# Kernel optimization log

Hardware: AMD Instinct MI355X
Metric: run time of the kernel (lower is better)

Reference implementation:

```python
import jax, jax.numpy as jnp
import numpy as np

NUM_GROUPS = 32
EPS = 1e-5


def setup_inputs() -> dict:
    key = jax.random.key(0)
    k1, k2, k3 = jax.random.split(key, 3)
    B, C, H, W = 16, 768, 32, 32
    x = jax.random.normal(k1, (B, C, H, W), dtype=jnp.float32)
    # 1x1-conv weights, scaled ~1/sqrt(fan_in) so softmax logits are sane
    w_qkv = jax.random.normal(k2, (3 * C, C), dtype=jnp.float32) / np.sqrt(C)
    b_qkv = jnp.zeros((3 * C,), dtype=jnp.float32)
    w_out = jax.random.normal(k3, (C, C), dtype=jnp.float32) / np.sqrt(C)
    b_out = jnp.zeros((C,), dtype=jnp.float32)
    gn_gamma = jnp.ones((C,), dtype=jnp.float32)
    gn_beta = jnp.zeros((C,), dtype=jnp.float32)
    return {"x": x, "gn_gamma": gn_gamma, "gn_beta": gn_beta,
            "w_qkv": w_qkv, "b_qkv": b_qkv, "w_out": w_out, "b_out": b_out}


def _group_norm(x, gamma, beta):
    B, C, H, W = x.shape
    G = NUM_GROUPS
    xr = x.reshape(B, G, C // G, H, W)
    mean = xr.mean(axis=(2, 3, 4), keepdims=True)
    var = xr.var(axis=(2, 3, 4), keepdims=True)  # biased, matches torch GroupNorm
    xn = ((xr - mean) * jax.lax.rsqrt(var + EPS)).reshape(B, C, H, W)
    return xn * gamma[None, :, None, None] + beta[None, :, None, None]


def reference(x, gn_gamma, gn_beta, w_qkv, b_qkv, w_out, b_out):
    B, C, H, W = x.shape
    res = x
    xn = _group_norm(x, gn_gamma, gn_beta)
    # 1x1 conv == channel GEMM: [B,3C,H,W]
    qkv = jnp.einsum('bchw,oc->bohw', xn, w_qkv) + b_qkv[None, :, None, None]
    q, k, v = jnp.split(qkv, 3, axis=1)
    hw = H * W
    q = q.reshape(B, C, hw)
    k = k.reshape(B, C, hw)
    v = v.reshape(B, C, hw)
    scale = hw ** -0.5
    # attention over the channel axis (C is 'seq len', hw is feature dim)
    att = jnp.einsum('bid,bjd->bij', q, k) * scale  # [B, C, C]
    att = jax.nn.softmax(att, axis=-1)
    # dropout p = 0.0 -> identity
    out = jnp.einsum('bij,bjd->bid', att, v).reshape(B, C, H, W)
    out = jnp.einsum('bchw,oc->bohw', out, w_out) + b_out[None, :, None, None]
    return out + res
```

## Files before the change

kernel.cpp:

```cpp
#include <hip/hip_runtime.h>
#include <hip/hip_bf16.h>

#define HW 1024
#define C_CH 768
#define BATCH 16
#define NG 32
#define CPG 24
#define EPS 1e-5f

typedef __attribute__((ext_vector_type(8))) short bf16x8;
typedef __attribute__((ext_vector_type(4))) float f32x4;
typedef unsigned short u16;
typedef unsigned int u32;

typedef const __attribute__((address_space(1))) void* gas_ptr;
typedef __attribute__((address_space(3))) void* las_ptr;

__device__ __forceinline__ void load_lds16(const void* g, void* l) {
    __builtin_amdgcn_global_load_lds((gas_ptr)g, (las_ptr)l, 16, 0, 0);
}

__device__ __forceinline__ u16 f2bf(float f) {
    __hip_bfloat16 h = __float2bfloat16(f);
    return *(u16*)&h;
}
__device__ __forceinline__ float bf2f(u16 u) {
    return __uint_as_float(((u32)u) << 16);
}

__device__ __forceinline__ void xcd_remap(int& bx, int& by, int& bz) {
    const int nbx = gridDim.x, nby = gridDim.y;
    const int nwg = nbx * nby * gridDim.z;
    int bid = blockIdx.x + nbx * (blockIdx.y + nby * blockIdx.z);
    if ((nwg & 7) == 0) {
        const int q = nwg >> 3;
        bid = (bid & 7) * q + (bid >> 3);
    }
    bx = bid % nbx;
    int t2 = bid / nbx;
    by = t2 % nby;
    bz = t2 / nby;
}

__global__ __launch_bounds__(256) void cast_bf16_kernel(const float4* __restrict__ in,
                                                        ushort4* __restrict__ out, int n4) {
    int i = blockIdx.x * 256 + threadIdx.x;
    if (i >= n4) return;
    float4 v = in[i];
    ushort4 u;
    u.x = f2bf(v.x); u.y = f2bf(v.y); u.z = f2bf(v.z); u.w = f2bf(v.w);
    out[i] = u;
}

__global__ __launch_bounds__(256) void gn_stats_kernel(const float* __restrict__ x,
                                                       float* __restrict__ stats) {
    int bg = blockIdx.x;
    const float4* p4 = (const float4*)(x + (size_t)bg * (CPG * HW));
    float s = 0.f, s2 = 0.f;
    for (int i = threadIdx.x; i < (CPG * HW) / 4; i += 256) {
        float4 v = p4[i];
        s  += v.x + v.y + v.z + v.w;
        s2 += v.x * v.x + v.y * v.y + v.z * v.z + v.w * v.w;
    }
    int lane = threadIdx.x & 63, wid = threadIdx.x >> 6;
    for (int off = 32; off; off >>= 1) {
        s  += __shfl_xor(s,  off, 64);
        s2 += __shfl_xor(s2, off, 64);
    }
    __shared__ float red[8];
    if (lane == 0) { red[wid * 2] = s; red[wid * 2 + 1] = s2; }
    __syncthreads();
    if (threadIdx.x == 0) {
        s = red[0] + red[2] + red[4] + red[6];
        s2 = red[1] + red[3] + red[5] + red[7];
        float mean = s / (float)(CPG * HW);
        float var  = s2 / (float)(CPG * HW) - mean * mean;
        stats[2 * bg]     = mean;
        stats[2 * bg + 1] = rsqrtf(var + EPS);
    }
}

__global__ __launch_bounds__(256) void gn_norm_kernel(const float* __restrict__ x,
                                                      const float* __restrict__ stats,
                                                      const float* __restrict__ gamma,
                                                      const float* __restrict__ beta,
                                                      __hip_bfloat16* __restrict__ xnT) {
    __shared__ float lds[64][65];
    int b  = blockIdx.y;
    int p0 = blockIdx.x * 64;
    int t = threadIdx.x;
    int lane = t & 63;
    int grp  = t >> 6;
    for (int cc = 0; cc < C_CH / 64; cc++) {
        int c0 = cc * 64;
        for (int i = 0; i < 16; i++) {
            int c = c0 + grp * 16 + i;
            float2 st = ((const float2*)stats)[b * NG + c / CPG];
            float ga = gamma[c], be = beta[c];
            float v = x[((size_t)b * C_CH + c) * HW + p0 + lane];
            lds[lane][grp * 16 + i] = (v - st.x) * st.y * ga + be;
        }
        __syncthreads();
        for (int i = 0; i < 16; i++) {
            int pp = grp * 16 + i;
            xnT[((size_t)b * HW + p0 + pp) * C_CH + c0 + lane] =
                __float2bfloat16(lds[pp][lane]);
        }
        __syncthreads();
    }
}

__global__ __launch_bounds__(256) void softmax_kernel(__hip_bfloat16* __restrict__ att) {
    int row  = blockIdx.x * 4 + (threadIdx.x >> 6);
    int lane = threadIdx.x & 63;
    u16* p = (u16*)(att + (size_t)row * C_CH);
    float v[12];
    float m = -1e30f;
    for (int j = 0; j < 12; j++) {
        v[j] = bf2f(p[j * 64 + lane]);
        m = fmaxf(m, v[j]);
    }
    for (int off = 32; off; off >>= 1) m = fmaxf(m, __shfl_xor(m, off, 64));
    float s = 0.f;
    for (int j = 0; j < 12; j++) { v[j] = __expf(v[j] - m); s += v[j]; }
    for (int off = 32; off; off >>= 1) s += __shfl_xor(s, off, 64);
    float inv = 1.0f / s;
    for (int j = 0; j < 12; j++) p[j * 64 + lane] = f2bf(v[j] * inv);
}

template<int OUT_F32>
__global__ __launch_bounds__(256, 2) void gemm_nt_kernel(
    const __hip_bfloat16* __restrict__ A, long sA,
    const __hip_bfloat16* __restrict__ B, long sB,
    void* __restrict__ Cout, long sC, int ldc,
    int K, float scale,
    const float* __restrict__ bias_row,
    const float* __restrict__ bias_col,
    const float* __restrict__ residual, long sR)
{
    __shared__ __hip_bfloat16 ldsA[128 * 64];
    __shared__ __hip_bfloat16 ldsB[128 * 64];
    int bxx, byy, bzz;
    xcd_remap(bxx, byy, bzz);
    const int t  = threadIdx.x;
    const int b  = bzz;
    const int m0 = byy * 128;
    const int n0 = bxx * 128;
    const int lane = t & 63;
    const int wid  = t >> 6;
    const int wm = wid >> 1, wn = wid & 1;
    const int lrow = lane & 15, lk = lane >> 4;

    const int srow   = t >> 3;
    const int schunk = t & 7;
    const int kphys  = (schunk ^ (srow & 7)) * 8;

    const __hip_bfloat16* aBase = A + (size_t)b * sA + (size_t)(m0 + srow) * K + kphys;
    const __hip_bfloat16* bBase = B + (size_t)b * sB + (size_t)(n0 + srow) * K + kphys;
    const int ldsDst = (t & ~63) * 8;

    f32x4 acc[4][4] = {};

    const int nk = K >> 6;
    for (int kt = 0; kt < nk; kt++) {
        __syncthreads();
        const __hip_bfloat16* ak = aBase + (size_t)kt * 64;
        const __hip_bfloat16* bk = bBase + (size_t)kt * 64;
        for (int r = 0; r < 4; r++)
            load_lds16(ak + (size_t)r * 32 * K, &ldsA[ldsDst + r * 2048]);
        for (int r = 0; r < 4; r++)
            load_lds16(bk + (size_t)r * 32 * K, &ldsB[ldsDst + r * 2048]);
        __syncthreads();
        for (int h = 0; h < 2; h++) {
            bf16x8 af[4], bfr[4];
            const int lc = h * 4 + lk;
            for (int i = 0; i < 4; i++) {
                int row = wm * 64 + i * 16 + lrow;
                int pc = lc ^ (row & 7);
                af[i] = *(const bf16x8*)&ldsA[row * 64 + pc * 8];
            }
            for (int i = 0; i < 4; i++) {
                int col = wn * 64 + i * 16 + lrow;
                int pc = lc ^ (col & 7);
                bfr[i] = *(const bf16x8*)&ldsB[col * 64 + pc * 8];
            }
            for (int i = 0; i < 4; i++)
                for (int j = 0; j < 4; j++)
                    acc[i][j] = __builtin_amdgcn_mfma_f32_16x16x32_bf16(
                        af[i], bfr[j], acc[i][j], 0, 0, 0);
        }
    }

    __hip_bfloat16* outB = (__hip_bfloat16*)Cout;
    float* outF = (float*)Cout;
    for (int i = 0; i < 4; i++)
        for (int j = 0; j < 4; j++) {
            int row = m0 + wm * 64 + i * 16 + lk * 4;
            int col = n0 + wn * 64 + j * 16 + lrow;
            f32x4 a = acc[i][j];
            for (int r = 0; r < 4; r++) {
                int rr = row + r;
                float v = a[r] * scale;
                if (bias_row) v += bias_row[rr];
                if (bias_col) v += bias_col[col];
                if (residual) v += residual[(size_t)b * sR + (size_t)rr * ldc + col];
                size_t off = (size_t)b * sC + (size_t)rr * ldc + col;
                if (OUT_F32) outF[off] = v;
                else         outB[off] = __float2bfloat16(v);
            }
        }
}

__global__ __launch_bounds__(512, 2) void gemm_nt_qkv(
    const __hip_bfloat16* __restrict__ A,
    const __hip_bfloat16* __restrict__ B, long sB,
    __hip_bfloat16* __restrict__ Cout, long sC, int ldc,
    int K,
    const float* __restrict__ bias_row,
    __hip_bfloat16* __restrict__ vt_out, long sVT, int vt_start)
{
    __shared__ __hip_bfloat16 ldsA[256 * 64];
    __shared__ __hip_bfloat16 ldsB[128 * 64];
    int bxx, byy, bzz;
    xcd_remap(bxx, byy, bzz);
    const int t  = threadIdx.x;
    const int b  = bzz;
    const int m0 = byy * 256;
    const int n0 = bxx * 128;
    const int lane = t & 63;
    const int wid  = t >> 6;
    const int wm = wid >> 1;
    const int wn = wid & 1;
    const int lrow = lane & 15, lk = lane >> 4;

    const int srow  = t >> 3;
    const int kphys = ((t & 7) ^ (srow & 7)) * 8;
    const int dstW  = (t & ~63) * 8;

    const __hip_bfloat16* aBase = A + (size_t)(m0 + srow) * K + kphys;
    const __hip_bfloat16* bBase = B + (size_t)b * sB + (size_t)(n0 + srow) * K + kphys;

    f32x4 acc[4][4] = {};

    const int nk = K >> 6;
    for (int kt = 0; kt < nk; kt++) {
        __syncthreads();
        const __hip_bfloat16* ak = aBase + (size_t)kt * 64;
        const __hip_bfloat16* bk = bBase + (size_t)kt * 64;
#pragma unroll
        for (int l = 0; l < 4; l++)
            load_lds16(ak + (size_t)l * 64 * K, &ldsA[dstW + l * 4096]);
#pragma unroll
        for (int l = 0; l < 2; l++)
            load_lds16(bk + (size_t)l * 64 * K, &ldsB[dstW + l * 4096]);
        __syncthreads();
#pragma unroll
        for (int h = 0; h < 2; h++) {
            bf16x8 af[4], bfr[4];
            const int lc = h * 4 + lk;
#pragma unroll
            for (int i = 0; i < 4; i++) {
                int row = wm * 64 + i * 16 + lrow;
                af[i] = *(const bf16x8*)&ldsA[row * 64 + (lc ^ (row & 7)) * 8];
            }
#pragma unroll
            for (int j = 0; j < 4; j++) {
                int col = wn * 64 + j * 16 + lrow;
                bfr[j] = *(const bf16x8*)&ldsB[col * 64 + (lc ^ (col & 7)) * 8];
            }
#pragma unroll
            for (int i = 0; i < 4; i++)
#pragma unroll
                for (int j = 0; j < 4; j++)
                    acc[i][j] = __builtin_amdgcn_mfma_f32_16x16x32_bf16(
                        af[i], bfr[j], acc[i][j], 0, 0, 0);
        }
    }

    if (m0 >= vt_start) {
        __hip_bfloat16* vtp = vt_out + (size_t)b * sVT;
#pragma unroll
        for (int i = 0; i < 4; i++)
#pragma unroll
            for (int j = 0; j < 4; j++) {
                int row = m0 + wm * 64 + i * 16 + lk * 4;
                int col = n0 + wn * 64 + j * 16 + lrow;
                f32x4 a = acc[i][j];
                ushort4 u;
                u.x = f2bf(a[0] + bias_row[row + 0]);
                u.y = f2bf(a[1] + bias_row[row + 1]);
                u.z = f2bf(a[2] + bias_row[row + 2]);
                u.w = f2bf(a[3] + bias_row[row + 3]);
                *(ushort4*)(vtp + (size_t)col * C_CH + (row - vt_start)) = u;
            }
        return;
    }

#pragma unroll
    for (int i = 0; i < 4; i++)
#pragma unroll
        for (int j = 0; j < 4; j++) {
            int row = m0 + wm * 64 + i * 16 + lk * 4;
            int col = n0 + wn * 64 + j * 16 + lrow;
            f32x4 a = acc[i][j];
#pragma unroll
            for (int r = 0; r < 4; r++) {
                int rr = row + r;
                Cout[(size_t)b * sC + (size_t)rr * ldc + col] =
                    __float2bfloat16(a[r] + bias_row[rr]);
            }
        }
}

extern "C" void kernel_launch(void* const* d_in, const int* in_sizes, int n_in,
                              void* d_out, int out_size, void* d_ws, size_t ws_size,
                              hipStream_t stream) {
    const float* x     = (const float*)d_in[0];
    const float* gamma = (const float*)d_in[1];
    const float* beta  = (const float*)d_in[2];
    const float* w_qkv = (const float*)d_in[3];
    const float* b_qkv = (const float*)d_in[4];
    const float* w_out = (const float*)d_in[5];
    const float* b_out = (const float*)d_in[6];

    char* ws = (char*)d_ws;
    size_t off = 0;
    auto alloc = [&](size_t bytes) {
        void* p = ws + off;
        off += (bytes + 255) & ~(size_t)255;
        return p;
    };
    __hip_bfloat16* xnT   = (__hip_bfloat16*)alloc((size_t)BATCH * HW * C_CH * 2);
    __hip_bfloat16* wqkvB = (__hip_bfloat16*)alloc((size_t)3 * C_CH * C_CH * 2);
    __hip_bfloat16* woutB = (__hip_bfloat16*)alloc((size_t)C_CH * C_CH * 2);
    __hip_bfloat16* qk    = (__hip_bfloat16*)alloc((size_t)BATCH * 2 * C_CH * HW * 2);
    __hip_bfloat16* vT    = (__hip_bfloat16*)alloc((size_t)BATCH * HW * C_CH * 2);
    __hip_bfloat16* att   = (__hip_bfloat16*)alloc((size_t)BATCH * C_CH * C_CH * 2);
    __hip_bfloat16* outT  = (__hip_bfloat16*)alloc((size_t)BATCH * HW * C_CH * 2);
    float* stats          = (float*)alloc((size_t)BATCH * NG * 2 * 4);

    {
        int n4 = (3 * C_CH * C_CH) / 4;
        cast_bf16_kernel<<<(n4 + 255) / 256, 256, 0, stream>>>(
            (const float4*)w_qkv, (ushort4*)wqkvB, n4);
        int n4b = (C_CH * C_CH) / 4;
        cast_bf16_kernel<<<(n4b + 255) / 256, 256, 0, stream>>>(
            (const float4*)w_out, (ushort4*)woutB, n4b);
    }
    gn_stats_kernel<<<BATCH * NG, 256, 0, stream>>>(x, stats);
    gn_norm_kernel<<<dim3(HW / 64, BATCH), 256, 0, stream>>>(x, stats, gamma, beta, xnT);

    gemm_nt_qkv<<<dim3(HW / 128, 2304 / 256, BATCH), 512, 0, stream>>>(
        wqkvB, xnT, (long)HW * C_CH, qk, (long)2 * C_CH * HW, HW,
        C_CH, b_qkv, vT, (long)HW * C_CH, 2 * C_CH);

    gemm_nt_kernel<0><<<dim3(C_CH / 128, C_CH / 128, BATCH), 256, 0, stream>>>(
        qk, (long)2 * C_CH * HW, qk + (size_t)C_CH * HW, (long)2 * C_CH * HW,
        att, (long)C_CH * C_CH, C_CH,
        HW, 1.0f / 32.0f, nullptr, nullptr, nullptr, 0);

    softmax_kernel<<<(BATCH * C_CH) / 4, 256, 0, stream>>>(att);

    gemm_nt_kernel<0><<<dim3(C_CH / 128, HW / 128, BATCH), 256, 0, stream>>>(
        vT, (long)HW * C_CH, att, (long)C_CH * C_CH, outT, (long)HW * C_CH, C_CH,
        C_CH, 1.0f, nullptr, nullptr, nullptr, 0);

    gemm_nt_kernel<1><<<dim3(HW / 128, C_CH / 128, BATCH), 256, 0, stream>>>(
        woutB, 0, outT, (long)HW * C_CH, (float*)d_out, (long)C_CH * HW, HW,
        C_CH, 1.0f, b_out, nullptr, x, (long)C_CH * HW);
}
```

Before: 228.2 us.

## Fuse GroupNorm stats and normalize/transposes into one LDS-staged kernel

Replaces the two-pass GroupNorm (stats kernel, then normalize+transpose kernel) with a single kernel per (batch, group). Each block stages the group's 24x1024 slab in LDS while accumulating sums, computes mean/rstd, then writes the normalized bf16 transposed output from LDS. This removes the second full read of x and one launch. In exchange each block holds about 98KB of LDS, which limits occupancy, and the grid is only 512 blocks.

```diff
diff --git a/kernel.cpp b/kernel.cpp
--- a/kernel.cpp
+++ b/kernel.cpp
@@ -52,61 +52,67 @@
     out[i] = u;
 }
 
-__global__ __launch_bounds__(256) void gn_stats_kernel(const float* __restrict__ x,
-                                                       float* __restrict__ stats) {
-    int bg = blockIdx.x;
-    const float4* p4 = (const float4*)(x + (size_t)bg * (CPG * HW));
+__global__ __launch_bounds__(512) void gn_fused_kernel(const float* __restrict__ x,
+                                                       const float* __restrict__ gamma,
+                                                       const float* __restrict__ beta,
+                                                       __hip_bfloat16* __restrict__ xnT) {
+    __shared__ float lds[24 * 1025];
+    __shared__ float red[18];
+    __shared__ float lga[24], lbe[24];
+    const int bg = blockIdx.x;
+    const int b = bg >> 5, g = bg & 31;
+    const int t = threadIdx.x;
+    const float4* src = (const float4*)(x + (size_t)bg * (CPG * HW));
+
     float s = 0.f, s2 = 0.f;
-    for (int i = threadIdx.x; i < (CPG * HW) / 4; i += 256) {
-        float4 v = p4[i];
+#pragma unroll 4
+    for (int i = 0; i < 12; i++) {
+        int fl4 = i * 512 + t;
+        float4 v = src[fl4];
+        int flat = fl4 * 4;
+        int c = flat >> 10, p = flat & 1023;
+        float* d = &lds[c * 1025 + p];
+        d[0] = v.x; d[1] = v.y; d[2] = v.z; d[3] = v.w;
         s  += v.x + v.y + v.z + v.w;
         s2 += v.x * v.x + v.y * v.y + v.z * v.z + v.w * v.w;
     }
-    int lane = threadIdx.x & 63, wid = threadIdx.x >> 6;
+    const int lane = t & 63, wid = t >> 6;
     for (int off = 32; off; off >>= 1) {
         s  += __shfl_xor(s,  off, 64);
         s2 += __shfl_xor(s2, off, 64);
     }
-    __shared__ float red[8];
     if (lane == 0) { red[wid * 2] = s; red[wid * 2 + 1] = s2; }
     __syncthreads();
-    if (threadIdx.x == 0) {
-        s = red[0] + red[2] + red[4] + red[6];
-        s2 = red[1] + red[3] + red[5] + red[7];
-        float mean = s / (float)(CPG * HW);
-        float var  = s2 / (float)(CPG * HW) - mean * mean;
-        stats[2 * bg]     = mean;
-        stats[2 * bg + 1] = rsqrtf(var + EPS);
-    }
-}
-
-__global__ __launch_bounds__(256) void gn_norm_kernel(const float* __restrict__ x,
-                                                      const float* __restrict__ stats,
-                                                      const float* __restrict__ gamma,
-                                                      const float* __restrict__ beta,
-                                                      __hip_bfloat16* __restrict__ xnT) {
-    __shared__ float lds[64][65];
-    int b  = blockIdx.y;
-    int p0 = blockIdx.x * 64;
-    int t = threadIdx.x;
-    int lane = t & 63;
-    int grp  = t >> 6;
-    for (int cc = 0; cc < C_CH / 64; cc++) {
-        int c0 = cc * 64;
-        for (int i = 0; i < 16; i++) {
-            int c = c0 + grp * 16 + i;
-            float2 st = ((const float2*)stats)[b * NG + c / CPG];
-            float ga = gamma[c], be = beta[c];
-            float v = x[((size_t)b * C_CH + c) * HW + p0 + lane];
-            lds[lane][grp * 16 + i] = (v - st.x) * st.y * ga + be;
-        }
-        __syncthreads();
-        for (int i = 0; i < 16; i++) {
-            int pp = grp * 16 + i;
-            xnT[((size_t)b * HW + p0 + pp) * C_CH + c0 + lane] =
-                __float2bfloat16(lds[pp][lane]);
-        }
-        __syncthreads();
+    if (t == 0) {
+        float ts = 0.f, ts2 = 0.f;
+        for (int w = 0; w < 8; w++) { ts += red[w * 2]; ts2 += red[w * 2 + 1]; }
+        float mean = ts / (float)(CPG * HW);
+        float var  = ts2 / (float)(CPG * HW) - mean * mean;
+        red[16] = mean;
+        red[17] = rsqrtf(var + EPS);
+    }
+    __syncthreads();
+    const float mean = red[16], rstd = red[17];
+    const int cbase = g * CPG;
+    if (t < CPG) {
+        float a = gamma[cbase + t] * rstd;
+        lga[t] = a;
+        lbe[t] = beta[cbase + t] - mean * a;
+    }
+    __syncthreads();
+
+    u16* dst = (u16*)xnT + (size_t)b * HW * C_CH + cbase;
+#pragma unroll 4
+    for (int i = 0; i < 12; i++) {
+        int k = i * 512 + t;
+        int p = k / 6;
+        int c = (k - p * 6) * 4;
+        ushort4 u;
+        u.x = f2bf(lds[(c + 0) * 1025 + p] * lga[c + 0] + lbe[c + 0]);
+        u.y = f2bf(lds[(c + 1) * 1025 + p] * lga[c + 1] + lbe[c + 1]);
+        u.z = f2bf(lds[(c + 2) * 1025 + p] * lga[c + 2] + lbe[c + 2]);
+        u.w = f2bf(lds[(c + 3) * 1025 + p] * lga[c + 3] + lbe[c + 3]);
+        *(ushort4*)(dst + (size_t)p * C_CH + c) = u;
     }
 }
 
@@ -337,7 +343,6 @@
     __hip_bfloat16* vT    = (__hip_bfloat16*)alloc((size_t)BATCH * HW * C_CH * 2);
     __hip_bfloat16* att   = (__hip_bfloat16*)alloc((size_t)BATCH * C_CH * C_CH * 2);
     __hip_bfloat16* outT  = (__hip_bfloat16*)alloc((size_t)BATCH * HW * C_CH * 2);
-    float* stats          = (float*)alloc((size_t)BATCH * NG * 2 * 4);
 
     {
         int n4 = (3 * C_CH * C_CH) / 4;
@@ -347,8 +352,7 @@
         cast_bf16_kernel<<<(n4b + 255) / 256, 256, 0, stream>>>(
             (const float4*)w_out, (ushort4*)woutB, n4b);
     }
-    gn_stats_kernel<<<BATCH * NG, 256, 0, stream>>>(x, stats);
-    gn_norm_kernel<<<dim3(HW / 64, BATCH), 256, 0, stream>>>(x, stats, gamma, beta, xnT);
+    gn_fused_kernel<<<BATCH * NG, 512, 0, stream>>>(x, gamma, beta, xnT);
 
     gemm_nt_qkv<<<dim3(HW / 128, 2304 / 256, BATCH), 512, 0, stream>>>(
         wqkvB, xnT, (long)HW * C_CH, qk, (long)2 * C_CH * HW, HW,
```

New measurement: 206.2 us. 9.6% less time.
